# Kernel optimization log

Hardware: AMD Instinct MI355X
Metric: run time of the kernel (lower is better)

The kernel has to match this reference:

```python
import jax, jax.numpy as jnp
import numpy as np

TAU = 0.1          # temperature from init_kwargs
EPS = 1e-8         # torch.nn.CosineSimilarity default eps


def setup_inputs() -> dict:
    key = jax.random.key(0)
    k1, k2, k3 = jax.random.split(key, 3)
    B, D = 2048, 128
    return {
        "z_i": jax.random.normal(k1, (B, D), dtype=jnp.float32),
        "z_j": jax.random.normal(k2, (B, D), dtype=jnp.float32),
        "y": jax.random.randint(k3, (B,), 0, 10, dtype=jnp.int64),
    }


def reference(z_i, z_j, y):
    # p: (2N, D)
    p = jnp.concatenate([z_i, z_j], axis=0)
    n2 = p.shape[0]
    # Cosine similarity via norms + single GEMM (same math as pairwise
    # CosineSimilarity: dot / max(||a||*||b||, eps)), then temperature scale.
    norms = jnp.linalg.norm(p, axis=1)                      # (2N,)
    sim = (p @ p.T) / jnp.maximum(norms[:, None] * norms[None, :], EPS) / TAU

    # Positive mask: same label, diagonal removed.
    y2 = jnp.concatenate([y, y], axis=0)                    # (2N,)
    off_diag = 1.0 - jnp.eye(n2, dtype=sim.dtype)           # logit mask
    mask = (y2[:, None] == y2[None, :]).astype(sim.dtype) * off_diag

    # Masked log-softmax over each row (self excluded from denominator).
    exp_logits = jnp.exp(sim) * off_diag
    log_prob = sim - jnp.log(exp_logits.sum(axis=1, keepdims=True))

    mean_log_prob_pos = (mask * log_prob).sum(axis=1) / mask.sum(axis=1)
    return -mean_log_prob_pos.mean()
```

## Files before the change

kernel.cpp:

```cpp
#include <hip/hip_runtime.h>

#define N2 4096
#define D 128
#define TAU_INV 10.0f
#define E2SCALE 14.4269504088896340736f
#define JSL 8
#define ITL 32
#define GEMM_BLOCKS (ITL * JSL)
#define NT 16
#define NCLS 10
#define CGRP 16
#define CROWS (N2 / CGRP)
#define CB (NCLS * CGRP)

typedef __attribute__((ext_vector_type(8))) short bf16x8;
typedef __attribute__((ext_vector_type(16))) float floatx16;

__device__ __forceinline__ short f2bf(float f) {
    unsigned u = __float_as_uint(f);
    u = (u + 0x7fff + ((u >> 16) & 1)) >> 16;
    return (short)u;
}
__device__ __forceinline__ float bf2f(short s) {
    return __uint_as_float(((unsigned)(unsigned short)s) << 16);
}

__global__ __launch_bounds__(64) void prep_kernel(const float* __restrict__ zi,
                                                  const float* __restrict__ zj,
                                                  short* __restrict__ qb,
                                                  short* __restrict__ qb2,
                                                  float* __restrict__ se_g,
                                                  float* __restrict__ S) {
    int row = blockIdx.x;
    int lane = threadIdx.x;
    const float* src = (row < 2048) ? (zi + row * D) : (zj + (row - 2048) * D);
    float2 v = ((const float2*)src)[lane];
    float ss = v.x * v.x + v.y * v.y;
    #pragma unroll
    for (int m = 1; m < 64; m <<= 1) ss += __shfl_xor(ss, m);
    float inv = 1.0f / sqrtf(ss);
    short2 o;
    o.x = f2bf(v.x * inv);
    o.y = f2bf(v.y * inv);
    ((short2*)(qb + row * D))[lane] = o;
    int addr2 = (row >> 5) * 4096 + (lane >> 2) * 256 + (row & 31) * 8 + 2 * (lane & 3);
    *(short2*)(qb2 + addr2) = o;
    if (lane == 0) se_g[row] = 0.f;
    if (row == 0)
        for (int k = lane; k < NCLS * D + 2 * NCLS; k += 64) S[k] = 0.f;
}

__global__ __launch_bounds__(256) void main_kernel(const short* __restrict__ qb,
                                                   const short* __restrict__ qb2,
                                                   const long long* __restrict__ y,
                                                   float* __restrict__ se_g,
                                                   float* __restrict__ S) {
    int tid = threadIdx.x;
    int wave = tid >> 6;
    int lane = tid & 63;

    if (blockIdx.x >= GEMM_BLOCKS) {
        __shared__ float shS[256];
        __shared__ float shT[4];
        __shared__ float shC[2];
        int cb = blockIdx.x - GEMM_BLOCKS;
        int c  = cb / CGRP;
        int g  = cb % CGRP;
        int d  = tid & 127;
        int rh = tid >> 7;
        int r0 = g * CROWS + rh * (CROWS / 2);

        float sS = 0.f, sT = 0.f, cnt = 0.f;
        #pragma unroll 4
        for (int i = 0; i < CROWS / 2; ++i) {
            int r = r0 + i;
            bool m = ((int)y[r & 2047] == c);
            float q = bf2f(qb[r * D + d]);
            sS += m ? q : 0.f;
            sT += m ? q * q : 0.f;
            cnt += m ? 1.f : 0.f;
        }

        shS[tid] = sS;
        #pragma unroll
        for (int m = 1; m < 64; m <<= 1) sT += __shfl_xor(sT, m);
        if ((tid & 63) == 0) shT[tid >> 6] = sT;
        if (d == 0) shC[rh] = cnt;
        __syncthreads();
        if (tid < 128) atomicAdd(&S[c * D + tid], shS[tid] + shS[tid + 128]);
        if (tid == 0) {
            atomicAdd(&S[NCLS * D + c], shT[0] + shT[1] + shT[2] + shT[3]);
            atomicAdd(&S[NCLS * D + NCLS + c], shC[0] + shC[1]);
        }
        return;
    }

    int gb = blockIdx.x;
    int col  = lane & 31;
    int half = lane >> 5;
    int it = gb >> 3;
    int js = gb & (JSL - 1);
    int rbase = it * 128 + wave * 32;
    int jbase = js * 512;

    const short* ap = qb2 + ((rbase >> 5) * 4096) + lane * 8;
    bf16x8 af[8];
    #pragma unroll
    for (int k = 0; k < 8; ++k) af[k] = *(const bf16x8*)(ap + k * 512);

    float se[16];
    #pragma unroll
    for (int r = 0; r < 16; ++r) se[r] = 0.f;

    #pragma unroll
    for (int t = 0; t < NT; ++t) {
        int j0 = jbase + t * 32;
        const short* bp = qb2 + ((j0 >> 5) * 4096) + lane * 8;
        bf16x8 bf[8];
        #pragma unroll
        for (int k = 0; k < 8; ++k) bf[k] = *(const bf16x8*)(bp + k * 512);

        floatx16 acc;
        #pragma unroll
        for (int r = 0; r < 16; ++r) acc[r] = 0.f;
        #pragma unroll
        for (int k = 0; k < 8; ++k)
            acc = __builtin_amdgcn_mfma_f32_32x32x16_bf16(af[k], bf[k], acc, 0, 0, 0);

        if (j0 == rbase) {
            int jcol = j0 + col;
            #pragma unroll
            for (int r = 0; r < 16; ++r) {
                int rowr = rbase + (r & 3) + 8 * (r >> 2) + 4 * half;
                float e = __builtin_amdgcn_exp2f(acc[r] * E2SCALE);
                se[r] += (rowr == jcol) ? 0.f : e;
            }
        } else {
            #pragma unroll
            for (int r = 0; r < 16; ++r)
                se[r] += __builtin_amdgcn_exp2f(acc[r] * E2SCALE);
        }
    }

    #pragma unroll
    for (int r = 0; r < 16; ++r) {
        float a = se[r];
        #pragma unroll
        for (int m = 1; m < 32; m <<= 1) a += __shfl_xor(a, m);
        if (col == 0) {
            int rowr = rbase + (r & 3) + 8 * (r >> 2) + 4 * half;
            atomicAdd(&se_g[rowr], a);
        }
    }
}

__global__ __launch_bounds__(256) void finish_kernel(const float* __restrict__ se_g,
                                                     const float* __restrict__ S,
                                                     float* __restrict__ out) {
    int tid = threadIdx.x;
    int wave = tid >> 6;
    int lane = tid & 63;

    float P = 0.f;
    for (int c = wave; c < NCLS; c += 4) {
        float2 sv = ((const float2*)(S + c * D))[lane];
        float s2 = sv.x * sv.x + sv.y * sv.y;
        #pragma unroll
        for (int m = 1; m < 64; m <<= 1) s2 += __shfl_xor(s2, m);
        float n = S[NCLS * D + NCLS + c];
        P += (n >= 2.0f) ? (s2 - S[NCLS * D + c]) * TAU_INV / (n - 1.0f) : 0.f;
    }

    float L = 0.f;
    for (int i = tid; i < N2; i += 256) L += __logf(se_g[i]);
    #pragma unroll
    for (int m = 1; m < 64; m <<= 1) L += __shfl_xor(L, m);

    __shared__ float red[8];
    if (lane == 0) { red[wave] = L; red[4 + wave] = P; }
    __syncthreads();
    if (tid == 0) {
        float Ls = red[0] + red[1] + red[2] + red[3];
        float Ps = red[4] + red[5] + red[6] + red[7];
        out[0] = (Ls - Ps) * (1.0f / (float)N2);
    }
}

extern "C" void kernel_launch(void* const* d_in, const int* in_sizes, int n_in,
                              void* d_out, int out_size, void* d_ws, size_t ws_size,
                              hipStream_t stream) {
    const float*     zi = (const float*)d_in[0];
    const float*     zj = (const float*)d_in[1];
    const long long* y  = (const long long*)d_in[2];
    float* out = (float*)d_out;

    char* ws = (char*)d_ws;
    short* qb   = (short*)ws;
    short* qb2  = qb + N2 * D;
    float* se_g = (float*)(ws + 2 * N2 * D * sizeof(short));
    float* S    = se_g + N2;

    prep_kernel<<<N2, 64, 0, stream>>>(zi, zj, qb, qb2, se_g, S);
    main_kernel<<<GEMM_BLOCKS + CB, 256, 0, stream>>>(qb, qb2, y, se_g, S);
    finish_kernel<<<1, 256, 0, stream>>>(se_g, S, out);
}
```

Before: 87.96 us.

## Retile GEMM to 256x256 blocks with 8 waves and prefetch B fragments

Switches the fused similarity kernel to 512-thread blocks covering 256x256 tiles (256 GEMM blocks), and shortens each wave's column sweep to 8 tiles. It adds software prefetching of the next B fragment into registers, plus a block barrier each iteration that keeps the waves in lockstep so they share B loads through cache. The class-sum blocks are adapted to 8 waves. Risks are higher register pressure from double-buffered fragments, barrier stalls, and more atomics per row, because each row is now split across 16 column slices instead of 8.

```diff
diff --git a/kernel.cpp b/kernel.cpp
--- a/kernel.cpp
+++ b/kernel.cpp
@@ -4,10 +4,10 @@
 #define D 128
 #define TAU_INV 10.0f
 #define E2SCALE 14.4269504088896340736f
-#define JSL 8
-#define ITL 32
-#define GEMM_BLOCKS (ITL * JSL)
-#define NT 16
+#define BM 256
+#define BN 256
+#define NT (BN / 32)
+#define GEMM_BLOCKS ((N2 / BM) * (N2 / BN))
 #define NCLS 10
 #define CGRP 16
 #define CROWS (N2 / CGRP)
@@ -50,7 +50,7 @@
         for (int k = lane; k < NCLS * D + 2 * NCLS; k += 64) S[k] = 0.f;
 }
 
-__global__ __launch_bounds__(256) void main_kernel(const short* __restrict__ qb,
+__global__ __launch_bounds__(512) void main_kernel(const short* __restrict__ qb,
                                                    const short* __restrict__ qb2,
                                                    const long long* __restrict__ y,
                                                    float* __restrict__ se_g,
@@ -60,19 +60,19 @@
     int lane = tid & 63;
 
     if (blockIdx.x >= GEMM_BLOCKS) {
-        __shared__ float shS[256];
-        __shared__ float shT[4];
-        __shared__ float shC[2];
+        __shared__ float shS[512];
+        __shared__ float shT[8];
+        __shared__ float shC[4];
         int cb = blockIdx.x - GEMM_BLOCKS;
         int c  = cb / CGRP;
         int g  = cb % CGRP;
         int d  = tid & 127;
-        int rh = tid >> 7;
-        int r0 = g * CROWS + rh * (CROWS / 2);
+        int rg = tid >> 7;
+        int r0 = g * CROWS + rg * (CROWS / 4);
 
         float sS = 0.f, sT = 0.f, cnt = 0.f;
         #pragma unroll 4
-        for (int i = 0; i < CROWS / 2; ++i) {
+        for (int i = 0; i < CROWS / 4; ++i) {
             int r = r0 + i;
             bool m = ((int)y[r & 2047] == c);
             float q = bf2f(qb[r * D + d]);
@@ -84,13 +84,18 @@
         shS[tid] = sS;
         #pragma unroll
         for (int m = 1; m < 64; m <<= 1) sT += __shfl_xor(sT, m);
-        if ((tid & 63) == 0) shT[tid >> 6] = sT;
-        if (d == 0) shC[rh] = cnt;
+        if (lane == 0) shT[wave] = sT;
+        if (d == 0) shC[rg] = cnt;
         __syncthreads();
-        if (tid < 128) atomicAdd(&S[c * D + tid], shS[tid] + shS[tid + 128]);
+        if (tid < 128)
+            atomicAdd(&S[c * D + tid],
+                      shS[tid] + shS[tid + 128] + shS[tid + 256] + shS[tid + 384]);
         if (tid == 0) {
-            atomicAdd(&S[NCLS * D + c], shT[0] + shT[1] + shT[2] + shT[3]);
-            atomicAdd(&S[NCLS * D + NCLS + c], shC[0] + shC[1]);
+            float t8 = 0.f;
+            #pragma unroll
+            for (int w = 0; w < 8; ++w) t8 += shT[w];
+            atomicAdd(&S[NCLS * D + c], t8);
+            atomicAdd(&S[NCLS * D + NCLS + c], shC[0] + shC[1] + shC[2] + shC[3]);
         }
         return;
     }
@@ -98,10 +103,10 @@
     int gb = blockIdx.x;
     int col  = lane & 31;
     int half = lane >> 5;
-    int it = gb >> 3;
-    int js = gb & (JSL - 1);
-    int rbase = it * 128 + wave * 32;
-    int jbase = js * 512;
+    int it = gb >> 4;
+    int js = gb & 15;
+    int rbase = it * BM + wave * 32;
+    int jbase = js * BN;
 
     const short* ap = qb2 + ((rbase >> 5) * 4096) + lane * 8;
     bf16x8 af[8];
@@ -112,13 +117,25 @@
     #pragma unroll
     for (int r = 0; r < 16; ++r) se[r] = 0.f;
 
+    bf16x8 bf[8];
+    {
+        const short* bp = qb2 + ((jbase >> 5) * 4096) + lane * 8;
+        #pragma unroll
+        for (int k = 0; k < 8; ++k) bf[k] = *(const bf16x8*)(bp + k * 512);
+    }
+
     #pragma unroll
     for (int t = 0; t < NT; ++t) {
         int j0 = jbase + t * 32;
-        const short* bp = qb2 + ((j0 >> 5) * 4096) + lane * 8;
-        bf16x8 bf[8];
-        #pragma unroll
-        for (int k = 0; k < 8; ++k) bf[k] = *(const bf16x8*)(bp + k * 512);
+
+        __syncthreads();
+
+        bf16x8 bn[8];
+        if (t < NT - 1) {
+            const short* bp = qb2 + (((j0 + 32) >> 5) * 4096) + lane * 8;
+            #pragma unroll
+            for (int k = 0; k < 8; ++k) bn[k] = *(const bf16x8*)(bp + k * 512);
+        }
 
         floatx16 acc;
         #pragma unroll
@@ -139,6 +156,11 @@
             #pragma unroll
             for (int r = 0; r < 16; ++r)
                 se[r] += __builtin_amdgcn_exp2f(acc[r] * E2SCALE);
+        }
+
+        if (t < NT - 1) {
+            #pragma unroll
+            for (int k = 0; k < 8; ++k) bf[k] = bn[k];
         }
     }
 
@@ -201,6 +223,6 @@
     float* S    = se_g + N2;
 
     prep_kernel<<<N2, 64, 0, stream>>>(zi, zj, qb, qb2, se_g, S);
-    main_kernel<<<GEMM_BLOCKS + CB, 256, 0, stream>>>(qb, qb2, y, se_g, S);
+    main_kernel<<<GEMM_BLOCKS + CB, 512, 0, stream>>>(qb, qb2, y, se_g, S);
     finish_kernel<<<1, 256, 0, stream>>>(se_g, S, out);
 }
```

After: 89.08 us. Within noise of the previous version (+1.3%).
